# Optimization experiments

Measured on AMD Instinct MI355X. Metric: run time of the kernel, lower is better.

The kernel has to match this reference:

```python
import jax, jax.numpy as jnp
import numpy as np
import math

B, L, M, N, S = 1024, 32, 128, 4096, 32


def setup_inputs() -> dict:
    key = jax.random.key(0)
    k1, k2, k3 = jax.random.split(key, 3)
    k = jax.random.normal(k1, (B, L, M), dtype=jnp.float32)
    # kaiming-uniform-like init: U(-bound, bound)
    bound_e = math.sqrt(6.0 / (N * M))
    bound_d = math.sqrt(6.0 / (M * N))
    W_e = jax.random.uniform(k2, (L, N, M), dtype=jnp.float32, minval=-bound_e, maxval=bound_e)
    W_d = jax.random.uniform(k3, (L, M, N), dtype=jnp.float32, minval=-bound_d, maxval=bound_d)
    # decoder columns are unit-normalized along the m axis (dim=-2), as in __init__
    W_d = W_d / jnp.linalg.norm(W_d, axis=-2, keepdims=True)
    b_e = jnp.zeros((L, N), dtype=jnp.float32)
    b_d = jnp.zeros((L, M), dtype=jnp.float32)
    return {"k": k, "W_e": W_e, "b_e": b_e, "W_d": W_d, "b_d": b_d, "s": S}


def hard_thresholding(y, s):
    # keep the s largest-|.| activations per (batch, layer) row, zero the rest
    _, idx = jax.lax.top_k(jnp.abs(y), s)  # idx: [B, L, s]
    b, l, _ = y.shape
    mask = jnp.zeros_like(y).at[
        jnp.arange(b)[:, None, None], jnp.arange(l)[None, :, None], idx
    ].set(1.0)
    return y * mask


def reference(k, W_e, b_e, W_d, b_d, s):
    # NOTE: b_e is created by the module but (faithfully) unused in encode()
    k_bar = k - b_d                                  # [B, L, M]
    y = jnp.einsum('lnm,blm->bln', W_e, k_bar)        # [B, L, N]
    y = hard_thresholding(y, s)
    k_hat = jnp.einsum('lmn,bln->blm', W_d, y)        # [B, L, M]
    loss = jnp.mean((k_hat - k) ** 2)
    return (loss, k_hat, y)
```

## Files before the change

kernel.cpp:

```cpp
#include <hip/hip_runtime.h>
#include <hip/hip_bf16.h>

#define B_ 1024
#define L_ 32
#define M_ 128
#define N_ 4096
#define S_ 32
#define ROWS (B_ * L_)

typedef __attribute__((ext_vector_type(8))) short    short8_t;
typedef __attribute__((ext_vector_type(8))) unsigned short ushort8_t;
typedef __attribute__((ext_vector_type(4))) float    f32x4;

__device__ __forceinline__ unsigned short f2bf(float x) {
    unsigned u = __float_as_uint(x);
    unsigned r = (u + 0x7FFFu + ((u >> 16) & 1u)) >> 16;
    return (unsigned short)r;
}
__device__ __forceinline__ float bf2f(unsigned short h) {
    return __uint_as_float((unsigned)h << 16);
}

__global__ __launch_bounds__(256) void transpose_wd(const float* __restrict__ Wd,
                                                    float* __restrict__ WdT) {
    __shared__ float t[32][33];
    int l = blockIdx.z;
    int n0 = blockIdx.x * 32, m0 = blockIdx.y * 32;
    int tx = threadIdx.x & 31, ty = threadIdx.x >> 5;
    const float* src = Wd + (size_t)l * M_ * N_;
    for (int i = ty; i < 32; i += 8)
        t[i][tx] = src[(size_t)(m0 + i) * N_ + n0 + tx];
    __syncthreads();
    float* dst = WdT + (size_t)l * N_ * M_;
    for (int i = ty; i < 32; i += 8)
        dst[(size_t)(n0 + i) * M_ + m0 + tx] = t[tx][i];
}

__global__ __launch_bounds__(256) void zero_y_low(float* __restrict__ y) {
    const float4 z = {0.f, 0.f, 0.f, 0.f};
    int idx = blockIdx.x * 256 + threadIdx.x;
    for (int i = idx; i < ROWS * 512; i += 2048 * 256) {
        int row = i >> 9, slot = i & 511;
        reinterpret_cast<float4*>(y + (size_t)row * N_)[slot] = z;
    }
}

__global__ __launch_bounds__(256) void zero_y_high(float* __restrict__ y) {
    const float4 z = {0.f, 0.f, 0.f, 0.f};
    int idx = blockIdx.x * 256 + threadIdx.x;
    for (int i = idx; i < ROWS * 512; i += 2048 * 256) {
        int row = i >> 9, slot = i & 511;
        reinterpret_cast<float4*>(y + (size_t)row * N_ + 2048)[slot] = z;
    }
}

__global__ __launch_bounds__(256) void scatter_high(float* __restrict__ y,
                                                    const int* __restrict__ cidx,
                                                    const float* __restrict__ cval) {
    int g = blockIdx.x * 256 + threadIdx.x;
    int row = g >> 5;
    int n = cidx[g];
    if (n >= 2048) y[(size_t)row * N_ + n] = cval[g];
}

__global__ __launch_bounds__(256) void prep_w(const float* __restrict__ We,
                                              const float* __restrict__ bd,
                                              unsigned short* __restrict__ Wbf,
                                              float* __restrict__ cvec) {
    int l = blockIdx.y;
    int tid = threadIdx.x;
    int nl = tid >> 4, t = tid & 15;
    int n = blockIdx.x * 16 + nl;
    const float* w = We + ((size_t)l * N_ + n) * M_ + t * 8;
    const float* b = bd + l * M_ + t * 8;
    float4 w0 = *(const float4*)(w), w1 = *(const float4*)(w + 4);
    float4 b0 = *(const float4*)(b), b1 = *(const float4*)(b + 4);
    ushort8_t o;
    o[0] = f2bf(w0.x); o[1] = f2bf(w0.y); o[2] = f2bf(w0.z); o[3] = f2bf(w0.w);
    o[4] = f2bf(w1.x); o[5] = f2bf(w1.y); o[6] = f2bf(w1.z); o[7] = f2bf(w1.w);
    *reinterpret_cast<ushort8_t*>(Wbf + ((size_t)l * N_ + n) * 128 + t * 8) = o;
    float s = w0.x*b0.x + w0.y*b0.y + w0.z*b0.z + w0.w*b0.w
            + w1.x*b1.x + w1.y*b1.y + w1.z*b1.z + w1.w*b1.w;
    #pragma unroll
    for (int oo = 8; oo > 0; oo >>= 1) s += __shfl_xor(s, oo, 64);
    if (t == 0) cvec[(size_t)l * N_ + n] = s;
}

__global__ __launch_bounds__(256) void prep_a(const float* __restrict__ kin,
                                              unsigned short* __restrict__ Abf) {
    int g = blockIdx.x * 256 + threadIdx.x;
    int b = g >> 12, l = (g >> 7) & 31, m = g & 127;
    Abf[(((size_t)l * B_ + b) << 7) + m] = f2bf(kin[g]);
}

__device__ __forceinline__ int swz(int row) { return (row & 3) ^ ((row >> 2) & 3); }

#define CP 136

__global__ __launch_bounds__(256) void encoder_mfma(const unsigned short* __restrict__ Abf,
                                                    const unsigned short* __restrict__ Wbf,
                                                    const float* __restrict__ cvec,
                                                    unsigned short* __restrict__ y16) {
    const int l   = blockIdx.z;
    const int bn0 = blockIdx.x * 128;
    const int bm0 = blockIdx.y * 128;
    __shared__ __align__(16) unsigned short smem[128 * CP];
    unsigned short* As = smem;
    unsigned short* Bs = smem + 128 * 32;
    const int tid  = threadIdx.x;
    const int lane = tid & 63, wave = tid >> 6;
    const int wr = wave >> 1, wc = wave & 1;

    const unsigned short* Ab = Abf + (((size_t)l * B_ + bm0) << 7);
    const unsigned short* Wb = Wbf + (((size_t)l * N_ + bn0) << 7);

    auto stage = [&](int k0) {
        #pragma unroll
        for (int i = 0; i < 2; ++i) {
            int p   = i * 256 + tid;
            int row = p >> 2;
            int lc  = (p & 3) ^ swz(row);
            const unsigned short* g = Ab + ((size_t)row << 7) + k0 + lc * 8;
            unsigned dst = (unsigned)((i * 256 + (tid & ~63)) * 16);
            __builtin_amdgcn_global_load_lds(
                (const __attribute__((address_space(1))) void*)g,
                (__attribute__((address_space(3))) void*)((char*)As + dst), 16, 0, 0);
        }
        #pragma unroll
        for (int i = 0; i < 2; ++i) {
            int p   = i * 256 + tid;
            int row = p >> 2;
            int lc  = (p & 3) ^ swz(row);
            const unsigned short* g = Wb + ((size_t)row << 7) + k0 + lc * 8;
            unsigned dst = (unsigned)((i * 256 + (tid & ~63)) * 16);
            __builtin_amdgcn_global_load_lds(
                (const __attribute__((address_space(1))) void*)g,
                (__attribute__((address_space(3))) void*)((char*)Bs + dst), 16, 0, 0);
        }
    };

    f32x4 acc[4][4];
    #pragma unroll
    for (int i = 0; i < 4; ++i)
        #pragma unroll
        for (int j = 0; j < 4; ++j) acc[i][j] = (f32x4){0.f, 0.f, 0.f, 0.f};

    stage(0);
    __syncthreads();

    #pragma unroll
    for (int t = 0; t < 4; ++t) {
        short8_t aF[4], bF[4];
        const int kg = lane >> 4;
        #pragma unroll
        for (int mt = 0; mt < 4; ++mt) {
            int row = wr * 64 + mt * 16 + (lane & 15);
            int pc  = kg ^ swz(row);
            aF[mt] = *reinterpret_cast<const short8_t*>(As + row * 32 + pc * 8);
        }
        #pragma unroll
        for (int nt = 0; nt < 4; ++nt) {
            int row = wc * 64 + nt * 16 + (lane & 15);
            int pc  = kg ^ swz(row);
            bF[nt] = *reinterpret_cast<const short8_t*>(Bs + row * 32 + pc * 8);
        }
        #pragma unroll
        for (int mt = 0; mt < 4; ++mt)
            #pragma unroll
            for (int nt = 0; nt < 4; ++nt)
                acc[mt][nt] = __builtin_amdgcn_mfma_f32_16x16x32_bf16(
                    aF[mt], bF[nt], acc[mt][nt], 0, 0, 0);

        if (t < 3) {
            __syncthreads();
            stage((t + 1) * 32);
            __syncthreads();
        }
    }

    __syncthreads();

    #pragma unroll
    for (int nt = 0; nt < 4; ++nt) {
        int nl = wc * 64 + nt * 16 + (lane & 15);
        float cj = cvec[(size_t)l * N_ + bn0 + nl];
        #pragma unroll
        for (int mt = 0; mt < 4; ++mt) {
            #pragma unroll
            for (int j = 0; j < 4; ++j) {
                int rl = wr * 64 + mt * 16 + (lane >> 4) * 4 + j;
                smem[rl * CP + nl] = f2bf(acc[mt][nt][j] - cj);
            }
        }
    }
    __syncthreads();

    #pragma unroll
    for (int i = 0; i < 8; ++i) {
        int chunk = i * 256 + tid;
        int r = chunk >> 4, cch = chunk & 15;
        ushort8_t v = *reinterpret_cast<const ushort8_t*>(smem + r * CP + cch * 8);
        unsigned short* dst = y16 + ((size_t)((bm0 + r) * L_ + l)) * 8192 + 4096 + bn0 + cch * 8;
        *reinterpret_cast<ushort8_t*>(dst) = v;
    }
}

#define POOL 96
#define MARGIN 1.2e-3f

__global__ __launch_bounds__(256) void topk_decode(float* __restrict__ y,
                                                   const float* __restrict__ We,
                                                   const float* __restrict__ WdT,
                                                   const float* __restrict__ kin,
                                                   const float* __restrict__ cvec,
                                                   int* __restrict__ cidx,
                                                   float* __restrict__ cval,
                                                   float* __restrict__ khat,
                                                   float* __restrict__ partial) {
    const int w    = threadIdx.x >> 6;
    const int lane = threadIdx.x & 63;
    const int wid  = (blockIdx.x << 2) + w;
    const int l = wid >> 10, b = wid & 1023;
    const int row = b * L_ + l;

    __shared__ __align__(16) float kinS[4][M_];
    __shared__ int   pidxS[4][POOL];
    __shared__ float pexS[4][POOL];
    __shared__ int   sidxS[4][S_];
    __shared__ float svalS[4][S_];
    __shared__ int   pcntS[4];

    float* yo = y + (size_t)row * N_;
    const unsigned short* ya = (const unsigned short*)y + (size_t)row * 8192 + 4096;

    kinS[w][lane]      = kin[(size_t)row * M_ + lane];
    kinS[w][lane + 64] = kin[(size_t)row * M_ + lane + 64];
    if (lane == 0) pcntS[w] = 0;

    ushort8_t u[8];
    #pragma unroll
    for (int j = 0; j < 8; ++j)
        u[j] = *reinterpret_cast<const ushort8_t*>(ya + j * 512 + lane * 8);
    float a[64];
    #pragma unroll
    for (int j = 0; j < 8; ++j)
        #pragma unroll
        for (int e = 0; e < 8; ++e)
            a[j * 8 + e] = fabsf(bf2f(u[j][e]));

    float mx = 0.0f;
    #pragma unroll
    for (int i = 0; i < 64; ++i) mx = fmaxf(mx, a[i]);
    #pragma unroll
    for (int o = 32; o > 0; o >>= 1) mx = fmaxf(mx, __shfl_xor(mx, o, 64));

    float lo = 0.0f, hi = mx;
    int cl = N_;
    for (int it = 0; it < 30 && cl > 40; ++it) {
        float t = 0.5f * (lo + hi);
        int c = 0;
        #pragma unroll
        for (int i = 0; i < 64; ++i) c += (a[i] >= t) ? 1 : 0;
        #pragma unroll
        for (int o = 32; o > 0; o >>= 1) c += __shfl_xor(c, o, 64);
        if (c >= S_) { lo = t; cl = c; } else { hi = t; }
    }

    const float th = lo - MARGIN;
    #pragma unroll
    for (int j = 0; j < 8; ++j)
        #pragma unroll
        for (int e = 0; e < 8; ++e)
            if (a[j * 8 + e] >= th) {
                int p = atomicAdd(&pcntS[w], 1);
                if (p < POOL) pidxS[w][p] = j * 512 + lane * 8 + e;
            }
    __asm__ __volatile__("s_waitcnt lgkmcnt(0)" ::: "memory");
    int c = pcntS[w]; c = c < POOL ? c : POOL;

    if (lane < c) {
        int n = pidxS[w][lane];
        const float4* wp4 = reinterpret_cast<const float4*>(We + ((size_t)l * N_ + n) * M_);
        const float4* kp4 = reinterpret_cast<const float4*>(kinS[w]);
        float acc = -cvec[(size_t)l * N_ + n];
        #pragma unroll 8
        for (int m4 = 0; m4 < 32; ++m4) {
            float4 wv = wp4[m4], kv = kp4[m4];
            acc = fmaf(wv.x, kv.x, acc);
            acc = fmaf(wv.y, kv.y, acc);
            acc = fmaf(wv.z, kv.z, acc);
            acc = fmaf(wv.w, kv.w, acc);
        }
        pexS[w][lane] = acc;
    }
    if (lane + 64 < c) {
        int n = pidxS[w][lane + 64];
        const float4* wp4 = reinterpret_cast<const float4*>(We + ((size_t)l * N_ + n) * M_);
        const float4* kp4 = reinterpret_cast<const float4*>(kinS[w]);
        float acc = -cvec[(size_t)l * N_ + n];
        #pragma unroll 8
        for (int m4 = 0; m4 < 32; ++m4) {
            float4 wv = wp4[m4], kv = kp4[m4];
            acc = fmaf(wv.x, kv.x, acc);
            acc = fmaf(wv.y, kv.y, acc);
            acc = fmaf(wv.z, kv.z, acc);
            acc = fmaf(wv.w, kv.w, acc);
        }
        pexS[w][lane + 64] = acc;
    }
    __asm__ __volatile__("s_waitcnt lgkmcnt(0)" ::: "memory");

    for (int e = lane; e < c; e += 64) {
        float ae = fabsf(pexS[w][e]);
        int   ne = pidxS[w][e];
        int rank = 0;
        for (int j = 0; j < c; ++j) {
            float aj = fabsf(pexS[w][j]);
            rank += ((aj > ae) || (aj == ae && pidxS[w][j] < ne)) ? 1 : 0;
        }
        if (rank < S_) {
            sidxS[w][rank] = ne;
            svalS[w][rank] = pexS[w][e];
        }
    }
    __asm__ __volatile__("s_waitcnt lgkmcnt(0)" ::: "memory");

    if (lane < S_) {
        int n = sidxS[w][lane];
        float v = svalS[w][lane];
        cidx[(size_t)row * S_ + lane] = n;
        cval[(size_t)row * S_ + lane] = v;
        if (n < 2048) yo[n] = v;
    }

    const float* wt = WdT + (size_t)l * N_ * M_;
    float acc0 = 0.0f, acc1 = 0.0f;
    #pragma unroll 4
    for (int j = 0; j < S_; ++j) {
        float v = svalS[w][j];
        const float* wrp = wt + (size_t)sidxS[w][j] * M_;
        acc0 = fmaf(v, wrp[lane], acc0);
        acc1 = fmaf(v, wrp[lane + 64], acc1);
    }
    khat[(size_t)row * M_ + lane]      = acc0;
    khat[(size_t)row * M_ + lane + 64] = acc1;
    float r0 = acc0 - kinS[w][lane];
    float r1 = acc1 - kinS[w][lane + 64];
    float s = r0 * r0 + r1 * r1;
    #pragma unroll
    for (int o = 32; o > 0; o >>= 1) s += __shfl_xor(s, o, 64);
    if (lane == 0) partial[row] = s;
}

__global__ __launch_bounds__(256) void reduce_loss(const float* __restrict__ partial,
                                                   float* __restrict__ out_loss) {
    __shared__ float red[256];
    int tid = threadIdx.x;
    float s = 0.0f;
    for (int i = tid; i < ROWS / 4; i += 256) {
        float4 v = reinterpret_cast<const float4*>(partial)[i];
        s += v.x + v.y + v.z + v.w;
    }
    red[tid] = s;
    __syncthreads();
    for (int off = 128; off > 0; off >>= 1) {
        if (tid < off) red[tid] += red[tid + off];
        __syncthreads();
    }
    if (tid == 0) out_loss[0] = red[0] / (float)((size_t)B_ * L_ * M_);
}

extern "C" void kernel_launch(void* const* d_in, const int* in_sizes, int n_in,
                              void* d_out, int out_size, void* d_ws, size_t ws_size,
                              hipStream_t stream) {
    const float* kin = (const float*)d_in[0];
    const float* We  = (const float*)d_in[1];
    const float* Wd  = (const float*)d_in[3];
    const float* bd  = (const float*)d_in[4];

    float* out   = (float*)d_out;
    float* loss  = out;
    float* khat  = out + 1;
    float* y_out = out + 1 + (size_t)B_ * L_ * M_;

    char* ws = (char*)d_ws;
    unsigned short* Wbf = (unsigned short*)ws;
    float*          WdT = (float*)ws;
    unsigned short* Abf = (unsigned short*)(ws + (64u << 20));
    int*   cidx    = (int*)  (ws + (72u << 20));
    float* cval    = (float*)(ws + (76u << 20));
    float* cvec    = (float*)(ws + (80u << 20));
    float* partial = (float*)(ws + (81u << 20));

    zero_y_low<<<2048, 256, 0, stream>>>(y_out);
    prep_w<<<dim3(N_ / 16, L_), 256, 0, stream>>>(We, bd, Wbf, cvec);
    prep_a<<<(B_ * L_ * M_) / 256, 256, 0, stream>>>(kin, Abf);
    encoder_mfma<<<dim3(N_ / 128, B_ / 128, L_), 256, 0, stream>>>(
        Abf, Wbf, cvec, (unsigned short*)y_out);
    transpose_wd<<<dim3(N_ / 32, M_ / 32, L_), 256, 0, stream>>>(Wd, WdT);
    topk_decode<<<ROWS / 4, 256, 0, stream>>>(y_out, We, WdT, kin, cvec,
                                              cidx, cval, khat, partial);
    zero_y_high<<<2048, 256, 0, stream>>>(y_out);
    scatter_high<<<(ROWS * S_) / 256, 256, 0, stream>>>(y_out, cidx, cval);
    reduce_loss<<<1, 256, 0, stream>>>(partial, loss);
}
```

Before: 600.8 us.

## Fuse y zeroing and top-k scatter into topk_decode with dense row writes

```diff
diff --git a/kernel.cpp b/kernel.cpp
--- a/kernel.cpp
+++ b/kernel.cpp
@@ -34,33 +34,6 @@
     float* dst = WdT + (size_t)l * N_ * M_;
     for (int i = ty; i < 32; i += 8)
         dst[(size_t)(n0 + i) * M_ + m0 + tx] = t[tx][i];
-}
-
-__global__ __launch_bounds__(256) void zero_y_low(float* __restrict__ y) {
-    const float4 z = {0.f, 0.f, 0.f, 0.f};
-    int idx = blockIdx.x * 256 + threadIdx.x;
-    for (int i = idx; i < ROWS * 512; i += 2048 * 256) {
-        int row = i >> 9, slot = i & 511;
-        reinterpret_cast<float4*>(y + (size_t)row * N_)[slot] = z;
-    }
-}
-
-__global__ __launch_bounds__(256) void zero_y_high(float* __restrict__ y) {
-    const float4 z = {0.f, 0.f, 0.f, 0.f};
-    int idx = blockIdx.x * 256 + threadIdx.x;
-    for (int i = idx; i < ROWS * 512; i += 2048 * 256) {
-        int row = i >> 9, slot = i & 511;
-        reinterpret_cast<float4*>(y + (size_t)row * N_ + 2048)[slot] = z;
-    }
-}
-
-__global__ __launch_bounds__(256) void scatter_high(float* __restrict__ y,
-                                                    const int* __restrict__ cidx,
-                                                    const float* __restrict__ cval) {
-    int g = blockIdx.x * 256 + threadIdx.x;
-    int row = g >> 5;
-    int n = cidx[g];
-    if (n >= 2048) y[(size_t)row * N_ + n] = cval[g];
 }
 
 __global__ __launch_bounds__(256) void prep_w(const float* __restrict__ We,
@@ -205,7 +178,7 @@
     }
 }
 
-#define POOL 96
+#define POOL 128
 #define MARGIN 1.2e-3f
 
 __global__ __launch_bounds__(256) void topk_decode(float* __restrict__ y,
@@ -213,8 +186,6 @@
                                                    const float* __restrict__ WdT,
                                                    const float* __restrict__ kin,
                                                    const float* __restrict__ cvec,
-                                                   int* __restrict__ cidx,
-                                                   float* __restrict__ cval,
                                                    float* __restrict__ khat,
                                                    float* __restrict__ partial) {
     const int w    = threadIdx.x >> 6;
@@ -224,17 +195,20 @@
     const int row = b * L_ + l;
 
     __shared__ __align__(16) float kinS[4][M_];
-    __shared__ int   pidxS[4][POOL];
-    __shared__ float pexS[4][POOL];
-    __shared__ int   sidxS[4][S_];
-    __shared__ float svalS[4][S_];
-    __shared__ int   pcntS[4];
+    __shared__ int      pidxS[4][POOL];
+    __shared__ float    pexS[4][POOL];
+    __shared__ int      sidxS[4][S_];
+    __shared__ float    svalS[4][S_];
+    __shared__ unsigned maskS[4][128];
+    __shared__ int      pcntS[4];
 
     float* yo = y + (size_t)row * N_;
     const unsigned short* ya = (const unsigned short*)y + (size_t)row * 8192 + 4096;
 
     kinS[w][lane]      = kin[(size_t)row * M_ + lane];
     kinS[w][lane + 64] = kin[(size_t)row * M_ + lane + 64];
+    maskS[w][lane & 127] = 0u;
+    maskS[w][64 + lane]  = 0u;
     if (lane == 0) pcntS[w] = 0;
 
     ushort8_t u[8];
@@ -248,16 +222,31 @@
         for (int e = 0; e < 8; ++e)
             a[j * 8 + e] = fabsf(bf2f(u[j][e]));
 
-    float mx = 0.0f;
-    #pragma unroll
-    for (int i = 0; i < 64; ++i) mx = fmaxf(mx, a[i]);
-    #pragma unroll
-    for (int o = 32; o > 0; o >>= 1) mx = fmaxf(mx, __shfl_xor(mx, o, 64));
+    float mx = 0.0f, s1 = 0.0f, s2 = 0.0f;
+    #pragma unroll
+    for (int i = 0; i < 64; ++i) {
+        mx = fmaxf(mx, a[i]);
+        s1 += a[i];
+        s2 = fmaf(a[i], a[i], s2);
+    }
+    #pragma unroll
+    for (int o = 32; o > 0; o >>= 1) {
+        mx = fmaxf(mx, __shfl_xor(mx, o, 64));
+        s1 += __shfl_xor(s1, o, 64);
+        s2 += __shfl_xor(s2, o, 64);
+    }
+    const float mu  = s1 * (1.0f / 4096.0f);
+    const float var = fmaxf(s2 * (1.0f / 4096.0f) - mu * mu, 0.0f);
+    const float sg  = sqrtf(var);
 
     float lo = 0.0f, hi = mx;
     int cl = N_;
-    for (int it = 0; it < 30 && cl > 40; ++it) {
-        float t = 0.5f * (lo + hi);
+    for (int it = 0; it < 30 && cl > 48; ++it) {
+        float t;
+        if      (it == 0) t = mu + 2.20f * sg;
+        else if (it == 1) t = mu + 2.96f * sg;
+        else              t = 0.5f * (lo + hi);
+        t = fminf(fmaxf(t, lo), hi);
         int c = 0;
         #pragma unroll
         for (int i = 0; i < 64; ++i) c += (a[i] >= t) ? 1 : 0;
@@ -327,10 +316,24 @@
 
     if (lane < S_) {
         int n = sidxS[w][lane];
-        float v = svalS[w][lane];
-        cidx[(size_t)row * S_ + lane] = n;
-        cval[(size_t)row * S_ + lane] = v;
-        if (n < 2048) yo[n] = v;
+        atomicOr(&maskS[w][n >> 5], 1u << (n & 31));
+    }
+    __asm__ __volatile__("s_waitcnt lgkmcnt(0)" ::: "memory");
+
+    #pragma unroll
+    for (int i = 0; i < 16; ++i) {
+        int slot = i * 64 + lane;
+        unsigned wm = maskS[w][slot >> 3];
+        unsigned bits = (wm >> ((slot & 7) * 4)) & 0xFu;
+        float4 v = {0.f, 0.f, 0.f, 0.f};
+        if (bits) {
+            #pragma unroll 4
+            for (int j = 0; j < S_; ++j) {
+                int n = sidxS[w][j];
+                if ((n >> 2) == slot) reinterpret_cast<float*>(&v)[n & 3] = svalS[w][j];
+            }
+        }
+        *reinterpret_cast<float4*>(yo + slot * 4) = v;
     }
 
     const float* wt = WdT + (size_t)l * N_ * M_;
@@ -387,20 +390,15 @@
     unsigned short* Wbf = (unsigned short*)ws;
     float*          WdT = (float*)ws;
     unsigned short* Abf = (unsigned short*)(ws + (64u << 20));
-    int*   cidx    = (int*)  (ws + (72u << 20));
-    float* cval    = (float*)(ws + (76u << 20));
     float* cvec    = (float*)(ws + (80u << 20));
     float* partial = (float*)(ws + (81u << 20));
 
-    zero_y_low<<<2048, 256, 0, stream>>>(y_out);
     prep_w<<<dim3(N_ / 16, L_), 256, 0, stream>>>(We, bd, Wbf, cvec);
     prep_a<<<(B_ * L_ * M_) / 256, 256, 0, stream>>>(kin, Abf);
     encoder_mfma<<<dim3(N_ / 128, B_ / 128, L_), 256, 0, stream>>>(
         Abf, Wbf, cvec, (unsigned short*)y_out);
     transpose_wd<<<dim3(N_ / 32, M_ / 32, L_), 256, 0, stream>>>(Wd, WdT);
     topk_decode<<<ROWS / 4, 256, 0, stream>>>(y_out, We, WdT, kin, cvec,
-                                              cidx, cval, khat, partial);
-    zero_y_high<<<2048, 256, 0, stream>>>(y_out);
-    scatter_high<<<(ROWS * S_) / 256, 256, 0, stream>>>(y_out, cidx, cval);
+                                              khat, partial);
     reduce_loss<<<1, 256, 0, stream>>>(partial, loss);
 }
```

Result: slower. 681.9 us (+13.5%).
